# Kernel tuning notes

Hardware: AMD Instinct MI355X
Metric: run time of the kernel (lower is better)

## Reference

```python
import jax, jax.numpy as jnp
import numpy as np
from functools import partial

ZONEOUT = 0.1  # eval-mode zoneout: h = h_new + zr*(h_prev - h_new)


def gru_layer(x, h0, kernel, recurrent, bias, zr):
    """Keras v2 GRU (reset_after=True), gate order [z, r, h].
    x: [B,T,D], h0: [B,U], kernel: [D,3U], recurrent: [U,3U], bias: [2,3U].
    Returns pre-zoneout outputs [B,T,U]; zoneout applies only to the carried state."""
    U = h0.shape[-1]
    b_in, b_rec = bias[0], bias[1]
    # precompute input projection for all timesteps (the compute-heavy GEMM)
    xw = jnp.einsum('btd,dk->btk', x, kernel) + b_in  # [B,T,3U]

    def step(h, xw_t):
        m = h @ recurrent + b_rec                      # [B,3U]
        xz, xr, xh = xw_t[:, :U], xw_t[:, U:2 * U], xw_t[:, 2 * U:]
        mz, mr, mh = m[:, :U], m[:, U:2 * U], m[:, 2 * U:]
        z = jax.nn.sigmoid(xz + mz)
        r = jax.nn.sigmoid(xr + mr)
        hh = jnp.tanh(xh + r * mh)
        h_new = z * h + (1.0 - z) * hh                 # cell output
        h_carry = h_new + zr * (h - h_new)             # eval zoneout on state
        return h_carry, h_new

    _, ys = jax.lax.scan(step, h0, jnp.swapaxes(xw, 0, 1))  # scan over T
    return jnp.swapaxes(ys, 0, 1)  # [B,T,U]


def setup_inputs() -> dict:
    key = jax.random.key(0)
    ks = jax.random.split(key, 16)
    B, T, D, U = 32, 1024, 256, 512
    s_in, s_rec = 1.0 / np.sqrt(D), 1.0 / np.sqrt(U)
    return {
        'x':   jax.random.normal(ks[0], (B, T, D), jnp.float32),
        'k0':  jax.random.normal(ks[1], (D, 3 * U), jnp.float32) * s_in,
        'r0':  jax.random.normal(ks[2], (U, 3 * U), jnp.float32) * s_rec,
        'b0':  jnp.zeros((2, 3 * U), jnp.float32),
        'ks':  jax.random.normal(ks[3], (U, 3 * U), jnp.float32) * s_rec,
        'rs':  jax.random.normal(ks[4], (U, 3 * U), jnp.float32) * s_rec,
        'bs':  jnp.zeros((2, 3 * U), jnp.float32),
        'h00': jax.random.normal(ks[5], (1, U), jnp.float32),
        'h01': jax.random.normal(ks[6], (1, U), jnp.float32),
        'h02': jax.random.normal(ks[7], (1, U), jnp.float32),
        'a':   jnp.ones((3,), jnp.float32),  # scalar skip multipliers a_11, a_12, a_22
        'wd':  jax.random.normal(ks[8], (U, D), jnp.float32) * s_rec,
        'bd':  jnp.zeros((D,), jnp.float32),
    }


def reference(x, k0, r0, b0, ks, rs, bs, h00, h01, h02, a, wd, bd):
    B = x.shape[0]
    tile = lambda h: jnp.tile(h, (B, 1))  # learnable init state -> batch
    # layer 0
    out0 = gru_layer(x, tile(h00), k0, r0, b0, ZONEOUT)
    # RK-style skip connections with a SHARED cell but per-layer learnable init states
    h0_skip = [tile(h01), tile(h02)]
    intermediates = []
    x_cur = out0
    idx = 0
    for i in range(2):  # num_skip_connections = num_rnn_layers - 1 = 2
        pred = gru_layer(x_cur, h0_skip[i], ks, rs, bs, ZONEOUT)
        intermediates.append(pred)
        x_cur = out0
        for j in range(i + 1):
            x_cur = x_cur + a[idx] * intermediates[j]
            idx += 1
    # dense output head (linear)
    return jnp.einsum('btu,ud->btd', x_cur, wd) + bd
```

## Files before the change

### kernel.cpp

```cpp
#include <hip/hip_runtime.h>

typedef __attribute__((ext_vector_type(8))) short short8;
typedef __attribute__((ext_vector_type(4))) float f32x4;
typedef __attribute__((ext_vector_type(4))) unsigned short u16x4;
typedef unsigned short ushort;
typedef unsigned long long ull;

#define MFMA16(a,b,c) __builtin_amdgcn_mfma_f32_16x16x32_bf16((a),(b),(c),0,0,0)

static __device__ __forceinline__ float bf2f(ushort u){
  union { unsigned int i; float f; } z; z.i = ((unsigned int)u) << 16; return z.f;
}
static __device__ __forceinline__ ushort f2bf(float f){
  union { float f; unsigned int i; } z; z.f = f;
  unsigned int x = z.i;
  unsigned int r = (x + 0x7fffu + ((x >> 16) & 1u)) >> 16;
  return (ushort)r;
}

static __device__ __forceinline__ float ld_ring_bf(const ushort* base, int idx){
  const unsigned int* p = (const unsigned int*)(base + (idx & ~1));
  unsigned int w = __hip_atomic_load(p, __ATOMIC_RELAXED, __HIP_MEMORY_SCOPE_AGENT);
  return bf2f((idx & 1) ? (ushort)(w >> 16) : (ushort)(w & 0xffffu));
}
static __device__ __forceinline__ void st_hc2(ushort* p, ushort v){
  unsigned int vv = v;
  asm volatile("global_store_short %0, %1, off sc0 sc1" :: "v"(p), "v"(vv) : "memory");
}
static __device__ __forceinline__ void st_hc8(ushort* p, ull v){
  asm volatile("global_store_dwordx2 %0, %1, off sc0 sc1" :: "v"(p), "v"(v) : "memory");
}

static __device__ __forceinline__ void ld_frag16(const ushort* p, short8* o){
  asm volatile(
    "global_load_dwordx4 %0, %16, off sc0 sc1\n\t"
    "global_load_dwordx4 %1, %16, off offset:64 sc0 sc1\n\t"
    "global_load_dwordx4 %2, %16, off offset:128 sc0 sc1\n\t"
    "global_load_dwordx4 %3, %16, off offset:192 sc0 sc1\n\t"
    "global_load_dwordx4 %4, %16, off offset:256 sc0 sc1\n\t"
    "global_load_dwordx4 %5, %16, off offset:320 sc0 sc1\n\t"
    "global_load_dwordx4 %6, %16, off offset:384 sc0 sc1\n\t"
    "global_load_dwordx4 %7, %16, off offset:448 sc0 sc1\n\t"
    "global_load_dwordx4 %8, %16, off offset:512 sc0 sc1\n\t"
    "global_load_dwordx4 %9, %16, off offset:576 sc0 sc1\n\t"
    "global_load_dwordx4 %10, %16, off offset:640 sc0 sc1\n\t"
    "global_load_dwordx4 %11, %16, off offset:704 sc0 sc1\n\t"
    "global_load_dwordx4 %12, %16, off offset:768 sc0 sc1\n\t"
    "global_load_dwordx4 %13, %16, off offset:832 sc0 sc1\n\t"
    "global_load_dwordx4 %14, %16, off offset:896 sc0 sc1\n\t"
    "global_load_dwordx4 %15, %16, off offset:960 sc0 sc1\n\t"
    "s_waitcnt vmcnt(0)"
    : "=&v"(o[0]), "=&v"(o[1]), "=&v"(o[2]), "=&v"(o[3]),
      "=&v"(o[4]), "=&v"(o[5]), "=&v"(o[6]), "=&v"(o[7]),
      "=&v"(o[8]), "=&v"(o[9]), "=&v"(o[10]), "=&v"(o[11]),
      "=&v"(o[12]), "=&v"(o[13]), "=&v"(o[14]), "=&v"(o[15])
    : "v"(p)
    : "memory");
  __builtin_amdgcn_sched_barrier(0);
}

static __device__ __forceinline__ void ld_frag32(const ushort* pa, const ushort* pb,
                                                 short8* oa, short8* ob){
  asm volatile(
    "global_load_dwordx4 %0, %32, off sc0 sc1\n\t"
    "global_load_dwordx4 %1, %32, off offset:64 sc0 sc1\n\t"
    "global_load_dwordx4 %2, %32, off offset:128 sc0 sc1\n\t"
    "global_load_dwordx4 %3, %32, off offset:192 sc0 sc1\n\t"
    "global_load_dwordx4 %4, %32, off offset:256 sc0 sc1\n\t"
    "global_load_dwordx4 %5, %32, off offset:320 sc0 sc1\n\t"
    "global_load_dwordx4 %6, %32, off offset:384 sc0 sc1\n\t"
    "global_load_dwordx4 %7, %32, off offset:448 sc0 sc1\n\t"
    "global_load_dwordx4 %8, %32, off offset:512 sc0 sc1\n\t"
    "global_load_dwordx4 %9, %32, off offset:576 sc0 sc1\n\t"
    "global_load_dwordx4 %10, %32, off offset:640 sc0 sc1\n\t"
    "global_load_dwordx4 %11, %32, off offset:704 sc0 sc1\n\t"
    "global_load_dwordx4 %12, %32, off offset:768 sc0 sc1\n\t"
    "global_load_dwordx4 %13, %32, off offset:832 sc0 sc1\n\t"
    "global_load_dwordx4 %14, %32, off offset:896 sc0 sc1\n\t"
    "global_load_dwordx4 %15, %32, off offset:960 sc0 sc1\n\t"
    "global_load_dwordx4 %16, %33, off sc0 sc1\n\t"
    "global_load_dwordx4 %17, %33, off offset:64 sc0 sc1\n\t"
    "global_load_dwordx4 %18, %33, off offset:128 sc0 sc1\n\t"
    "global_load_dwordx4 %19, %33, off offset:192 sc0 sc1\n\t"
    "global_load_dwordx4 %20, %33, off offset:256 sc0 sc1\n\t"
    "global_load_dwordx4 %21, %33, off offset:320 sc0 sc1\n\t"
    "global_load_dwordx4 %22, %33, off offset:384 sc0 sc1\n\t"
    "global_load_dwordx4 %23, %33, off offset:448 sc0 sc1\n\t"
    "global_load_dwordx4 %24, %33, off offset:512 sc0 sc1\n\t"
    "global_load_dwordx4 %25, %33, off offset:576 sc0 sc1\n\t"
    "global_load_dwordx4 %26, %33, off offset:640 sc0 sc1\n\t"
    "global_load_dwordx4 %27, %33, off offset:704 sc0 sc1\n\t"
    "global_load_dwordx4 %28, %33, off offset:768 sc0 sc1\n\t"
    "global_load_dwordx4 %29, %33, off offset:832 sc0 sc1\n\t"
    "global_load_dwordx4 %30, %33, off offset:896 sc0 sc1\n\t"
    "global_load_dwordx4 %31, %33, off offset:960 sc0 sc1\n\t"
    "s_waitcnt vmcnt(0)"
    : "=&v"(oa[0]), "=&v"(oa[1]), "=&v"(oa[2]), "=&v"(oa[3]),
      "=&v"(oa[4]), "=&v"(oa[5]), "=&v"(oa[6]), "=&v"(oa[7]),
      "=&v"(oa[8]), "=&v"(oa[9]), "=&v"(oa[10]), "=&v"(oa[11]),
      "=&v"(oa[12]), "=&v"(oa[13]), "=&v"(oa[14]), "=&v"(oa[15]),
      "=&v"(ob[0]), "=&v"(ob[1]), "=&v"(ob[2]), "=&v"(ob[3]),
      "=&v"(ob[4]), "=&v"(ob[5]), "=&v"(ob[6]), "=&v"(ob[7]),
      "=&v"(ob[8]), "=&v"(ob[9]), "=&v"(ob[10]), "=&v"(ob[11]),
      "=&v"(ob[12]), "=&v"(ob[13]), "=&v"(ob[14]), "=&v"(ob[15])
    : "v"(pa), "v"(pb)
    : "memory");
  __builtin_amdgcn_sched_barrier(0);
}

static __device__ __forceinline__ void ld_frag32s(
    const ushort* pa, const ushort* pb,
    const ushort* q0, const ushort* q1, const ushort* q2,
    const ushort* q3, const ushort* q4, const ushort* q5,
    short8* oa, short8* ob,
    unsigned int* s0, unsigned int* s1, ull* s2,
    unsigned int* s3, unsigned int* s4, ull* s5)
{
  asm volatile(
    "global_load_dwordx4 %0, %38, off sc0 sc1\n\t"
    "global_load_dwordx4 %1, %38, off offset:64 sc0 sc1\n\t"
    "global_load_dwordx4 %2, %38, off offset:128 sc0 sc1\n\t"
    "global_load_dwordx4 %3, %38, off offset:192 sc0 sc1\n\t"
    "global_load_dwordx4 %4, %38, off offset:256 sc0 sc1\n\t"
    "global_load_dwordx4 %5, %38, off offset:320 sc0 sc1\n\t"
    "global_load_dwordx4 %6, %38, off offset:384 sc0 sc1\n\t"
    "global_load_dwordx4 %7, %38, off offset:448 sc0 sc1\n\t"
    "global_load_dwordx4 %8, %38, off offset:512 sc0 sc1\n\t"
    "global_load_dwordx4 %9, %38, off offset:576 sc0 sc1\n\t"
    "global_load_dwordx4 %10, %38, off offset:640 sc0 sc1\n\t"
    "global_load_dwordx4 %11, %38, off offset:704 sc0 sc1\n\t"
    "global_load_dwordx4 %12, %38, off offset:768 sc0 sc1\n\t"
    "global_load_dwordx4 %13, %38, off offset:832 sc0 sc1\n\t"
    "global_load_dwordx4 %14, %38, off offset:896 sc0 sc1\n\t"
    "global_load_dwordx4 %15, %38, off offset:960 sc0 sc1\n\t"
    "global_load_dwordx4 %16, %39, off sc0 sc1\n\t"
    "global_load_dwordx4 %17, %39, off offset:64 sc0 sc1\n\t"
    "global_load_dwordx4 %18, %39, off offset:128 sc0 sc1\n\t"
    "global_load_dwordx4 %19, %39, off offset:192 sc0 sc1\n\t"
    "global_load_dwordx4 %20, %39, off offset:256 sc0 sc1\n\t"
    "global_load_dwordx4 %21, %39, off offset:320 sc0 sc1\n\t"
    "global_load_dwordx4 %22, %39, off offset:384 sc0 sc1\n\t"
    "global_load_dwordx4 %23, %39, off offset:448 sc0 sc1\n\t"
    "global_load_dwordx4 %24, %39, off offset:512 sc0 sc1\n\t"
    "global_load_dwordx4 %25, %39, off offset:576 sc0 sc1\n\t"
    "global_load_dwordx4 %26, %39, off offset:640 sc0 sc1\n\t"
    "global_load_dwordx4 %27, %39, off offset:704 sc0 sc1\n\t"
    "global_load_dwordx4 %28, %39, off offset:768 sc0 sc1\n\t"
    "global_load_dwordx4 %29, %39, off offset:832 sc0 sc1\n\t"
    "global_load_dwordx4 %30, %39, off offset:896 sc0 sc1\n\t"
    "global_load_dwordx4 %31, %39, off offset:960 sc0 sc1\n\t"
    "global_load_dword %32, %40, off sc0 sc1\n\t"
    "global_load_dword %33, %41, off sc0 sc1\n\t"
    "global_load_dwordx2 %34, %42, off sc0 sc1\n\t"
    "global_load_dword %35, %43, off sc0 sc1\n\t"
    "global_load_dword %36, %44, off sc0 sc1\n\t"
    "global_load_dwordx2 %37, %45, off sc0 sc1\n\t"
    "s_waitcnt vmcnt(0)"
    : "=&v"(oa[0]), "=&v"(oa[1]), "=&v"(oa[2]), "=&v"(oa[3]),
      "=&v"(oa[4]), "=&v"(oa[5]), "=&v"(oa[6]), "=&v"(oa[7]),
      "=&v"(oa[8]), "=&v"(oa[9]), "=&v"(oa[10]), "=&v"(oa[11]),
      "=&v"(oa[12]), "=&v"(oa[13]), "=&v"(oa[14]), "=&v"(oa[15]),
      "=&v"(ob[0]), "=&v"(ob[1]), "=&v"(ob[2]), "=&v"(ob[3]),
      "=&v"(ob[4]), "=&v"(ob[5]), "=&v"(ob[6]), "=&v"(ob[7]),
      "=&v"(ob[8]), "=&v"(ob[9]), "=&v"(ob[10]), "=&v"(ob[11]),
      "=&v"(ob[12]), "=&v"(ob[13]), "=&v"(ob[14]), "=&v"(ob[15]),
      "=&v"(*s0), "=&v"(*s1), "=&v"(*s2), "=&v"(*s3), "=&v"(*s4), "=&v"(*s5)
    : "v"(pa), "v"(pb), "v"(q0), "v"(q1), "v"(q2), "v"(q3), "v"(q4), "v"(q5)
    : "memory");
  __builtin_amdgcn_sched_barrier(0);
}

__global__ __launch_bounds__(256) void cvt_k(
    const float* __restrict__ in, ushort* __restrict__ out, int n)
{
  int i = (blockIdx.x * 256 + threadIdx.x) * 4;
  if (i < n){
    float4 v = *(const float4*)(in + i);
    u16x4 o = { f2bf(v.x), f2bf(v.y), f2bf(v.z), f2bf(v.w) };
    *(u16x4*)(out + i) = o;
  }
}

template<int F32OUT>
__global__ __launch_bounds__(256) void gemm_bias_k(
    const ushort* __restrict__ A,
    const ushort* __restrict__ B,
    const float*  __restrict__ bias,
    void* __restrict__ Cv,
    int M, int N, int K)
{
  __shared__ __align__(16) ushort Blds[64 * 40];
  const int tid  = threadIdx.x;
  const int wid  = tid >> 6;
  const int lane = tid & 63;
  const int quad = lane >> 4;
  const int lc   = lane & 15;
  const int nb   = N >> 6;
  const int bn   = (blockIdx.x % nb) << 6;
  const int bm   = (blockIdx.x / nb) << 6;

  const int sk  = tid >> 3;
  const int scg = tid & 7;

  f32x4 acc[4] = {{0,0,0,0},{0,0,0,0},{0,0,0,0},{0,0,0,0}};
  const int arow = bm + wid * 16 + lc;
  const ushort* aptr = A + (size_t)arow * K + quad * 8;

  for (int k0 = 0; k0 < K; k0 += 32){
    short8 bv = *(const short8*)(B + (size_t)(k0 + sk) * N + bn + (scg << 3));
    #pragma unroll
    for (int i = 0; i < 8; ++i){
      int c = (scg << 3) + i;
      int p = c * 40 + (((sk >> 3) ^ (scg & 3)) << 3) + (sk & 7);
      Blds[p] = (ushort)bv[i];
    }
    __syncthreads();
    short8 av = *(const short8*)(aptr + k0);
    #pragma unroll
    for (int nt = 0; nt < 4; ++nt){
      int c2 = (nt << 4) + lc;
      int p  = c2 * 40 + ((quad ^ ((c2 >> 3) & 3)) << 3);
      short8 bfrag = *(const short8*)(Blds + p);
      acc[nt] = MFMA16(av, bfrag, acc[nt]);
    }
    __syncthreads();
  }
  #pragma unroll
  for (int nt = 0; nt < 4; ++nt){
    #pragma unroll
    for (int i = 0; i < 4; ++i){
      int m = bm + wid * 16 + quad * 4 + i;
      int n = bn + (nt << 4) + lc;
      float v = acc[nt][i] + bias[n];
      if (F32OUT) ((float*)Cv)[(size_t)m * N + n] = v;
      else        ((ushort*)Cv)[(size_t)m * N + n] = f2bf(v);
    }
  }
}

#define NWG 96
#define RD 8
#define FSTEPS 1032

__global__ __launch_bounds__(384, 1) void rec3_k(
    const ushort* __restrict__ xw0,
    const ushort* __restrict__ R0b,
    const ushort* __restrict__ Ksb,
    const ushort* __restrict__ Rsb,
    const float*  __restrict__ b0v,
    const float*  __restrict__ bsv,
    const float*  __restrict__ h00,
    const float*  __restrict__ h01,
    const float*  __restrict__ h02,
    const float*  __restrict__ av,
    ushort* __restrict__ comb,
    ushort* __restrict__ rings,
    int* __restrict__ flags)
{
  __shared__ float m_lds[3][32][17];
  __shared__ float x_lds[3][32][17];
  __shared__ float bias_l[96];
  __shared__ __align__(16) ushort ks_lds[3 * 16 * 64 * 8];
  __shared__ __align__(16) ushort rs_lds[3 * 16 * 64 * 8];

  const int tid  = threadIdx.x;
  const int wid  = tid >> 6;
  const int lane = tid & 63;
  const int quad = lane >> 4;
  const int lc   = lane & 15;
  const int bid  = blockIdx.x;
  const int role = bid >> 5;
  const int g    = bid & 31;
  const int ug0  = g << 4;
  const int gate = wid % 3, mtile = wid / 3;
  const int col0 = (gate << 9) + ug0;

  ushort* h_ring    = rings + role * 131072;
  ushort* out0ring  = rings + 393216;
  ushort* pred0ring = rings + 524288;
  ushort* xw1ring   = rings + 655360;

  short8 bfragR[16];
  if (role == 0){
    #pragma unroll
    for (int f = 0; f < 16; ++f){
      short8 v;
      #pragma unroll
      for (int j = 0; j < 8; ++j)
        v[j] = (short)R0b[(size_t)(f * 32 + quad * 8 + j) * 1536 + col0 + lc];
      bfragR[f] = v;
    }
  }
  if (role > 0){
    if (mtile == 0){
      #pragma unroll
      for (int f = 0; f < 16; ++f){
        short8 v;
        #pragma unroll
        for (int j = 0; j < 8; ++j)
          v[j] = (short)Ksb[(size_t)(f * 32 + quad * 8 + j) * 1536 + col0 + lc];
        *(short8*)(ks_lds + (((gate << 4) + f) << 9) + (lane << 3)) = v;
      }
    } else {
      #pragma unroll
      for (int f = 0; f < 16; ++f){
        short8 v;
        #pragma unroll
        for (int j = 0; j < 8; ++j)
          v[j] = (short)Rsb[(size_t)(f * 32 + quad * 8 + j) * 1536 + col0 + lc];
        *(short8*)(rs_lds + (((gate << 4) + f) << 9) + (lane << 3)) = v;
      }
    }
  }
  const float* brec = ((role == 0) ? b0v : bsv) + 1536;
  if (tid < 48) bias_l[tid] = brec[(tid >> 4) * 512 + ug0 + (tid & 15)];
  if (tid >= 48 && tid < 96) bias_l[tid] = bsv[((tid - 48) >> 4) * 512 + ug0 + ((tid - 48) & 15)];
  const float a0 = av[0], a1 = av[1], a2 = av[2];
  const float* hinit = (role == 0) ? h00 : (role == 1) ? h01 : h02;

  const int  b0i  = tid >> 4;
  const int  u0   = tid & 15;
  const int  b1i  = (tid + 384) >> 4;
  const bool has1 = (tid < 128);
  const int  uu   = ug0 + u0;
  float hp0 = hinit[uu];
  float hp1 = hp0;

  ushort xz0 = 0, xr0 = 0, xh0 = 0, xz1 = 0, xr1 = 0, xh1 = 0;
  if (role == 0){
    size_t r0_ = ((size_t)b0i * 1024) * 1536 + uu;
    xz0 = xw0[r0_]; xr0 = xw0[r0_ + 512]; xh0 = xw0[r0_ + 1024];
    if (has1){
      size_t r1_ = ((size_t)b1i * 1024) * 1536 + uu;
      xz1 = xw0[r1_]; xr1 = xw0[r1_ + 512]; xh1 = xw0[r1_ + 1024];
    }
  }
  __syncthreads();

  long budget = 40000000L;
  for (int t = 0; t < 1024; ++t){
    const int s     = t + role;
    const int slot  = t & (RD - 1);
    const int pslot = (t - 1) & (RD - 1);

    ushort nz0 = 0, nr0 = 0, nh0 = 0, nz1 = 0, nr1 = 0, nh1 = 0;
    if (role == 0 && t < 1023){
      size_t r0_ = ((size_t)b0i * 1024 + t + 1) * 1536 + uu;
      nz0 = xw0[r0_]; nr0 = xw0[r0_ + 512]; nh0 = xw0[r0_ + 1024];
      if (has1){
        size_t r1_ = ((size_t)b1i * 1024 + t + 1) * 1536 + uu;
        nz1 = xw0[r1_]; nr1 = xw0[r1_ + 512]; nh1 = xw0[r1_ + 1024];
      }
    }

    {
      const bool needO = (t > 0);
      const bool needP = (role >= 1);
      const bool needF = (role <= 1) && (s >= RD);
      if ((needO || needP || needF) && wid == 0){
        const int  l    = lane & 31;
        const int* fo   = flags + (role * FSTEPS + (s - 1)) * 32 + l;
        const int* fp   = flags + ((role - 1) * FSTEPS + (s - 1)) * 32 + l;
        const int* ff   = flags + (2 * FSTEPS + (s - 6)) * 32 + l;
        while (budget > 0){
          bool ok = true;
          if (needO) ok &= (__hip_atomic_load(fo, __ATOMIC_RELAXED, __HIP_MEMORY_SCOPE_AGENT) != 0);
          if (needP) ok &= (__hip_atomic_load(fp, __ATOMIC_RELAXED, __HIP_MEMORY_SCOPE_AGENT) != 0);
          if (needF) ok &= (__hip_atomic_load(ff, __ATOMIC_RELAXED, __HIP_MEMORY_SCOPE_AGENT) != 0);
          if (__ballot(ok) == ~0ull) break;
          --budget;
        }
      }
      __syncthreads();
    }

    float o_s0 = 0, p_s0 = 0, x1z0 = 0, x1r0 = 0, x1h0 = 0;
    float o_s1 = 0, p_s1 = 0, x1z1 = 0, x1r1 = 0, x1h1 = 0;
    {
      short8 avm[16];
      short8 avx[16];
      const ushort* hr  = h_ring + pslot * 16384 + (mtile * 16 + lc) * 512 + quad * 8;
      const ushort* xr_ = ((role == 1) ? out0ring : pred0ring)
                        + slot * 16384 + (mtile * 16 + lc) * 512 + quad * 8;

      if (t == 0){
        #pragma unroll
        for (int f = 0; f < 16; ++f){
          short8 v;
          #pragma unroll
          for (int j = 0; j < 8; ++j)
            v[j] = (short)f2bf(hinit[f * 32 + quad * 8 + j]);
          avm[f] = v;
        }
        if (role >= 1) ld_frag16(xr_, avx);
        if (role == 2){
          int rb0 = slot * 16384 + b0i * 512 + uu;
          o_s0 = ld_ring_bf(out0ring, rb0);
          p_s0 = ld_ring_bf(pred0ring, rb0);
          ull xwp = __hip_atomic_load((const ull*)(xw1ring + (size_t)((slot * 32 + b0i) * 512 + uu) * 4),
                                      __ATOMIC_RELAXED, __HIP_MEMORY_SCOPE_AGENT);
          x1z0 = bf2f((ushort)(xwp & 0xffffu));
          x1r0 = bf2f((ushort)((xwp >> 16) & 0xffffu));
          x1h0 = bf2f((ushort)((xwp >> 32) & 0xffffu));
          if (has1){
            int rb1 = slot * 16384 + b1i * 512 + uu;
            o_s1 = ld_ring_bf(out0ring, rb1);
            p_s1 = ld_ring_bf(pred0ring, rb1);
            ull xwq = __hip_atomic_load((const ull*)(xw1ring + (size_t)((slot * 32 + b1i) * 512 + uu) * 4),
                                        __ATOMIC_RELAXED, __HIP_MEMORY_SCOPE_AGENT);
            x1z1 = bf2f((ushort)(xwq & 0xffffu));
            x1r1 = bf2f((ushort)((xwq >> 16) & 0xffffu));
            x1h1 = bf2f((ushort)((xwq >> 32) & 0xffffu));
          }
        }
      } else if (role == 0){
        ld_frag16(hr, avm);
      } else if (role == 1){
        ld_frag32(xr_, hr, avx, avm);
      } else {
        int rb0 = slot * 16384 + b0i * 512 + uu;
        int rb1 = slot * 16384 + b1i * 512 + uu;
        const ushort* q0 = out0ring  + (rb0 & ~1);
        const ushort* q1 = pred0ring + (rb0 & ~1);
        const ushort* q2 = xw1ring + (size_t)((slot * 32 + b0i) * 512 + uu) * 4;
        const ushort* q3 = has1 ? (out0ring  + (rb1 & ~1)) : q0;
        const ushort* q4 = has1 ? (pred0ring + (rb1 & ~1)) : q1;
        const ushort* q5 = has1 ? (xw1ring + (size_t)((slot * 32 + b1i) * 512 + uu) * 4) : q2;
        unsigned int w0, w1, w3, w4; ull w2, w5;
        ld_frag32s(xr_, hr, q0, q1, q2, q3, q4, q5,
                   avx, avm, &w0, &w1, &w2, &w3, &w4, &w5);
        int hi = uu & 1;
        o_s0 = bf2f(hi ? (ushort)(w0 >> 16) : (ushort)(w0 & 0xffffu));
        p_s0 = bf2f(hi ? (ushort)(w1 >> 16) : (ushort)(w1 & 0xffffu));
        x1z0 = bf2f((ushort)(w2 & 0xffffu));
        x1r0 = bf2f((ushort)((w2 >> 16) & 0xffffu));
        x1h0 = bf2f((ushort)((w2 >> 32) & 0xffffu));
        if (has1){
          o_s1 = bf2f(hi ? (ushort)(w3 >> 16) : (ushort)(w3 & 0xffffu));
          p_s1 = bf2f(hi ? (ushort)(w4 >> 16) : (ushort)(w4 & 0xffffu));
          x1z1 = bf2f((ushort)(w5 & 0xffffu));
          x1r1 = bf2f((ushort)((w5 >> 16) & 0xffffu));
          x1h1 = bf2f((ushort)((w5 >> 32) & 0xffffu));
        }
      }

      f32x4 am0 = {0,0,0,0}, am1 = {0,0,0,0};
      if (role == 0){
        #pragma unroll
        for (int f = 0; f < 16; ++f){
          if (f & 1) am1 = MFMA16(avm[f], bfragR[f], am1);
          else       am0 = MFMA16(avm[f], bfragR[f], am0);
        }
        f32x4 am = am0 + am1;
        #pragma unroll
        for (int i = 0; i < 4; ++i)
          m_lds[gate][(mtile << 4) + (quad << 2) + i][lc] = am[i];
      } else {
        f32x4 ax0 = {0,0,0,0}, ax1 = {0,0,0,0};
        #pragma unroll
        for (int f = 0; f < 16; ++f){
          short8 bx = *(const short8*)(ks_lds + (((gate << 4) + f) << 9) + (lane << 3));
          short8 br = *(const short8*)(rs_lds + (((gate << 4) + f) << 9) + (lane << 3));
          if (f & 1){ am1 = MFMA16(avm[f], br, am1); ax1 = MFMA16(avx[f], bx, ax1); }
          else      { am0 = MFMA16(avm[f], br, am0); ax0 = MFMA16(avx[f], bx, ax0); }
        }
        f32x4 am = am0 + am1, ax = ax0 + ax1;
        #pragma unroll
        for (int i = 0; i < 4; ++i){
          m_lds[gate][(mtile << 4) + (quad << 2) + i][lc] = am[i];
          x_lds[gate][(mtile << 4) + (quad << 2) + i][lc] = ax[i];
        }
      }
    }
    __syncthreads();

    ushort cb0 = 0, cb1 = 0;
    {
      int b = b0i;
      float mz = m_lds[0][b][u0] + bias_l[u0];
      float mr = m_lds[1][b][u0] + bias_l[16 + u0];
      float mh = m_lds[2][b][u0] + bias_l[32 + u0];
      float xz, xr, xh;
      if (role == 0){ xz = bf2f(xz0); xr = bf2f(xr0); xh = bf2f(xh0); }
      else if (role == 1){
        xz = x_lds[0][b][u0] + bias_l[48 + u0];
        xr = x_lds[1][b][u0] + bias_l[64 + u0];
        xh = x_lds[2][b][u0] + bias_l[80 + u0];
      } else {
        xz = x1z0 + a0 * x_lds[0][b][u0] + bias_l[48 + u0];
        xr = x1r0 + a0 * x_lds[1][b][u0] + bias_l[64 + u0];
        xh = x1h0 + a0 * x_lds[2][b][u0] + bias_l[80 + u0];
      }
      float z  = 1.f / (1.f + __expf(-(xz + mz)));
      float r  = 1.f / (1.f + __expf(-(xr + mr)));
      float axv = xh + r * mh;
      float hh = 1.f - 2.f / (1.f + __expf(2.f * axv));
      float hn = z * hp0 + (1.f - z) * hh;
      float hcv = hn + 0.1f * (hp0 - hn);
      hp0 = hcv;
      int rb = slot * 16384 + b * 512 + uu;
      st_hc2(h_ring + rb, f2bf(hcv));
      if (role == 0) st_hc2(out0ring + rb, f2bf(hn));
      else if (role == 1){
        st_hc2(pred0ring + rb, f2bf(hn));
        ull pv = (ull)f2bf(x_lds[0][b][u0])
               | ((ull)f2bf(x_lds[1][b][u0]) << 16)
               | ((ull)f2bf(x_lds[2][b][u0]) << 32);
        st_hc8(xw1ring + (size_t)((slot * 32 + b) * 512 + uu) * 4, pv);
      } else {
        cb0 = f2bf(o_s0 + a1 * p_s0 + a2 * hn);
      }
    }
    if (has1){
      int b = b1i;
      float mz = m_lds[0][b][u0] + bias_l[u0];
      float mr = m_lds[1][b][u0] + bias_l[16 + u0];
      float mh = m_lds[2][b][u0] + bias_l[32 + u0];
      float xz, xr, xh;
      if (role == 0){ xz = bf2f(xz1); xr = bf2f(xr1); xh = bf2f(xh1); }
      else if (role == 1){
        xz = x_lds[0][b][u0] + bias_l[48 + u0];
        xr = x_lds[1][b][u0] + bias_l[64 + u0];
        xh = x_lds[2][b][u0] + bias_l[80 + u0];
      } else {
        xz = x1z1 + a0 * x_lds[0][b][u0] + bias_l[48 + u0];
        xr = x1r1 + a0 * x_lds[1][b][u0] + bias_l[64 + u0];
        xh = x1h1 + a0 * x_lds[2][b][u0] + bias_l[80 + u0];
      }
      float z  = 1.f / (1.f + __expf(-(xz + mz)));
      float r  = 1.f / (1.f + __expf(-(xr + mr)));
      float axv = xh + r * mh;
      float hh = 1.f - 2.f / (1.f + __expf(2.f * axv));
      float hn = z * hp1 + (1.f - z) * hh;
      float hcv = hn + 0.1f * (hp1 - hn);
      hp1 = hcv;
      int rb = slot * 16384 + b * 512 + uu;
      st_hc2(h_ring + rb, f2bf(hcv));
      if (role == 0) st_hc2(out0ring + rb, f2bf(hn));
      else if (role == 1){
        st_hc2(pred0ring + rb, f2bf(hn));
        ull pv = (ull)f2bf(x_lds[0][b][u0])
               | ((ull)f2bf(x_lds[1][b][u0]) << 16)
               | ((ull)f2bf(x_lds[2][b][u0]) << 32);
        st_hc8(xw1ring + (size_t)((slot * 32 + b) * 512 + uu) * 4, pv);
      } else {
        cb1 = f2bf(o_s1 + a1 * p_s1 + a2 * hn);
      }
    }
    asm volatile("s_waitcnt vmcnt(0)" ::: "memory");
    __syncthreads();
    if (tid == 0)
      __hip_atomic_store(flags + (role * FSTEPS + s) * 32 + g, 1,
                         __ATOMIC_RELAXED, __HIP_MEMORY_SCOPE_AGENT);
    if (role == 2){
      comb[((size_t)b0i * 1024 + t) * 512 + uu] = cb0;
      if (has1) comb[((size_t)b1i * 1024 + t) * 512 + uu] = cb1;
    }

    if (role == 0){
      xz0 = nz0; xr0 = nr0; xh0 = nh0;
      xz1 = nz1; xr1 = nr1; xh1 = nh1;
    }
  }
}

extern "C" void kernel_launch(void* const* d_in, const int* in_sizes, int n_in,
                              void* d_out, int out_size, void* d_ws, size_t ws_size,
                              hipStream_t stream)
{
  const float* x   = (const float*)d_in[0];
  const float* k0  = (const float*)d_in[1];
  const float* r0  = (const float*)d_in[2];
  const float* b0  = (const float*)d_in[3];
  const float* ks  = (const float*)d_in[4];
  const float* rs  = (const float*)d_in[5];
  const float* bs  = (const float*)d_in[6];
  const float* h00 = (const float*)d_in[7];
  const float* h01 = (const float*)d_in[8];
  const float* h02 = (const float*)d_in[9];
  const float* a   = (const float*)d_in[10];
  const float* wd  = (const float*)d_in[11];
  const float* bd  = (const float*)d_in[12];
  float* outp = (float*)d_out;

  char* ws = (char*)d_ws;
  ushort* XW    = (ushort*)(ws);
  ushort* combp = (ushort*)(ws + 100663296u);
  ushort* xbf   = combp;
  ushort* rings = (ushort*)(ws + 134217728u);
  int*    flags = (int*)   (ws + 136577024u);
  ushort* k0b   = (ushort*)(ws + 136973312u);
  ushort* r0b   = (ushort*)(ws + 137759744u);
  ushort* ksb   = (ushort*)(ws + 139332608u);
  ushort* rsb   = (ushort*)(ws + 140905472u);
  ushort* wdb   = (ushort*)(ws + 142478336u);

  hipMemsetAsync(flags, 0, 3 * FSTEPS * 32 * sizeof(int), stream);

  dim3 blk(256);
  cvt_k<<<dim3(8192), blk, 0, stream>>>(x,  xbf, 8388608);
  cvt_k<<<dim3(384),  blk, 0, stream>>>(k0, k0b, 393216);
  cvt_k<<<dim3(768),  blk, 0, stream>>>(r0, r0b, 786432);
  cvt_k<<<dim3(768),  blk, 0, stream>>>(ks, ksb, 786432);
  cvt_k<<<dim3(768),  blk, 0, stream>>>(rs, rsb, 786432);
  cvt_k<<<dim3(128),  blk, 0, stream>>>(wd, wdb, 131072);

  gemm_bias_k<0><<<dim3(512 * 24), blk, 0, stream>>>(xbf, k0b, b0, XW, 32768, 1536, 256);
  rec3_k<<<dim3(NWG), dim3(384), 0, stream>>>(XW, r0b, ksb, rsb, b0, bs,
                                              h00, h01, h02, a, combp, rings, flags);
  gemm_bias_k<1><<<dim3(512 * 4), blk, 0, stream>>>(combp, wdb, bd, outp, 32768, 256, 512);
}
```

Before: 10.48 ms.

## Split recurrence flags into h-state and cross-layer sets, publish h early

The per-step flags change from one-shot booleans over all steps to monotonic step counters in a 64-entry ring, in two separate sets. One set signals that the carried h state is ready, the other that the cross-layer outputs (out0, pred0, xw1) are ready. Each workgroup now stores and publishes its h_ring slice first, then writes the cross-layer rings and raises a second flag, so same-role neighbours can start the next step sooner. All waves poll the flags instead of only wave 0, and the __syncthreads after the wait is removed. The cost is an extra vmcnt wait and barrier per step for roles 0 and 1, and reliance on every wave seeing the flags consistently without a barrier.

```diff
diff --git a/kernel.cpp b/kernel.cpp
--- a/kernel.cpp
+++ b/kernel.cpp
@@ -240,7 +240,6 @@
 
 #define NWG 96
 #define RD 8
-#define FSTEPS 1032
 
 __global__ __launch_bounds__(384, 1) void rec3_k(
     const ushort* __restrict__ xw0,
@@ -275,6 +274,9 @@
   const int gate = wid % 3, mtile = wid / 3;
   const int col0 = (gate << 9) + ug0;
 
+  int* flagsH = flags;
+  int* flagsX = flags + 6144;
+
   ushort* h_ring    = rings + role * 131072;
   ushort* out0ring  = rings + 393216;
   ushort* pred0ring = rings + 524288;
@@ -357,21 +359,20 @@
       const bool needO = (t > 0);
       const bool needP = (role >= 1);
       const bool needF = (role <= 1) && (s >= RD);
-      if ((needO || needP || needF) && wid == 0){
-        const int  l    = lane & 31;
-        const int* fo   = flags + (role * FSTEPS + (s - 1)) * 32 + l;
-        const int* fp   = flags + ((role - 1) * FSTEPS + (s - 1)) * 32 + l;
-        const int* ff   = flags + (2 * FSTEPS + (s - 6)) * 32 + l;
+      if (needO || needP || needF){
+        const int  l  = lane & 31;
+        const int* fo = flagsH + ((role << 6) + ((s - 1) & 63)) * 32 + l;
+        const int* fp = flagsX + (((role - 1) << 6) + ((s - 1) & 63)) * 32 + l;
+        const int* ff = flagsH + ((2 << 6) + ((s - 6) & 63)) * 32 + l;
         while (budget > 0){
           bool ok = true;
-          if (needO) ok &= (__hip_atomic_load(fo, __ATOMIC_RELAXED, __HIP_MEMORY_SCOPE_AGENT) != 0);
-          if (needP) ok &= (__hip_atomic_load(fp, __ATOMIC_RELAXED, __HIP_MEMORY_SCOPE_AGENT) != 0);
-          if (needF) ok &= (__hip_atomic_load(ff, __ATOMIC_RELAXED, __HIP_MEMORY_SCOPE_AGENT) != 0);
+          if (needO) ok &= (__hip_atomic_load(fo, __ATOMIC_RELAXED, __HIP_MEMORY_SCOPE_AGENT) >= s);
+          if (needP) ok &= (__hip_atomic_load(fp, __ATOMIC_RELAXED, __HIP_MEMORY_SCOPE_AGENT) >= s);
+          if (needF) ok &= (__hip_atomic_load(ff, __ATOMIC_RELAXED, __HIP_MEMORY_SCOPE_AGENT) >= s - 5);
           if (__ballot(ok) == ~0ull) break;
           --budget;
         }
       }
-      __syncthreads();
     }
 
     float o_s0 = 0, p_s0 = 0, x1z0 = 0, x1r0 = 0, x1h0 = 0;
@@ -474,6 +475,8 @@
     }
     __syncthreads();
 
+    float hn0v = 0.f, hn1v = 0.f;
+    ull   pv0 = 0, pv1 = 0;
     ushort cb0 = 0, cb1 = 0;
     {
       int b = b0i;
@@ -483,9 +486,11 @@
       float xz, xr, xh;
       if (role == 0){ xz = bf2f(xz0); xr = bf2f(xr0); xh = bf2f(xh0); }
       else if (role == 1){
-        xz = x_lds[0][b][u0] + bias_l[48 + u0];
-        xr = x_lds[1][b][u0] + bias_l[64 + u0];
-        xh = x_lds[2][b][u0] + bias_l[80 + u0];
+        float wz = x_lds[0][b][u0], wr = x_lds[1][b][u0], wh = x_lds[2][b][u0];
+        pv0 = (ull)f2bf(wz) | ((ull)f2bf(wr) << 16) | ((ull)f2bf(wh) << 32);
+        xz = wz + bias_l[48 + u0];
+        xr = wr + bias_l[64 + u0];
+        xh = wh + bias_l[80 + u0];
       } else {
         xz = x1z0 + a0 * x_lds[0][b][u0] + bias_l[48 + u0];
         xr = x1r0 + a0 * x_lds[1][b][u0] + bias_l[64 + u0];
@@ -497,19 +502,9 @@
       float hh = 1.f - 2.f / (1.f + __expf(2.f * axv));
       float hn = z * hp0 + (1.f - z) * hh;
       float hcv = hn + 0.1f * (hp0 - hn);
-      hp0 = hcv;
-      int rb = slot * 16384 + b * 512 + uu;
-      st_hc2(h_ring + rb, f2bf(hcv));
-      if (role == 0) st_hc2(out0ring + rb, f2bf(hn));
-      else if (role == 1){
-        st_hc2(pred0ring + rb, f2bf(hn));
-        ull pv = (ull)f2bf(x_lds[0][b][u0])
-               | ((ull)f2bf(x_lds[1][b][u0]) << 16)
-               | ((ull)f2bf(x_lds[2][b][u0]) << 32);
-        st_hc8(xw1ring + (size_t)((slot * 32 + b) * 512 + uu) * 4, pv);
-      } else {
-        cb0 = f2bf(o_s0 + a1 * p_s0 + a2 * hn);
-      }
+      hp0 = hcv; hn0v = hn;
+      st_hc2(h_ring + slot * 16384 + b * 512 + uu, f2bf(hcv));
+      if (role == 2) cb0 = f2bf(o_s0 + a1 * p_s0 + a2 * hn);
     }
     if (has1){
       int b = b1i;
@@ -519,9 +514,11 @@
       float xz, xr, xh;
       if (role == 0){ xz = bf2f(xz1); xr = bf2f(xr1); xh = bf2f(xh1); }
       else if (role == 1){
-        xz = x_lds[0][b][u0] + bias_l[48 + u0];
-        xr = x_lds[1][b][u0] + bias_l[64 + u0];
-        xh = x_lds[2][b][u0] + bias_l[80 + u0];
+        float wz = x_lds[0][b][u0], wr = x_lds[1][b][u0], wh = x_lds[2][b][u0];
+        pv1 = (ull)f2bf(wz) | ((ull)f2bf(wr) << 16) | ((ull)f2bf(wh) << 32);
+        xz = wz + bias_l[48 + u0];
+        xr = wr + bias_l[64 + u0];
+        xh = wh + bias_l[80 + u0];
       } else {
         xz = x1z1 + a0 * x_lds[0][b][u0] + bias_l[48 + u0];
         xr = x1r1 + a0 * x_lds[1][b][u0] + bias_l[64 + u0];
@@ -533,26 +530,38 @@
       float hh = 1.f - 2.f / (1.f + __expf(2.f * axv));
       float hn = z * hp1 + (1.f - z) * hh;
       float hcv = hn + 0.1f * (hp1 - hn);
-      hp1 = hcv;
-      int rb = slot * 16384 + b * 512 + uu;
-      st_hc2(h_ring + rb, f2bf(hcv));
-      if (role == 0) st_hc2(out0ring + rb, f2bf(hn));
-      else if (role == 1){
-        st_hc2(pred0ring + rb, f2bf(hn));
-        ull pv = (ull)f2bf(x_lds[0][b][u0])
-               | ((ull)f2bf(x_lds[1][b][u0]) << 16)
-               | ((ull)f2bf(x_lds[2][b][u0]) << 32);
-        st_hc8(xw1ring + (size_t)((slot * 32 + b) * 512 + uu) * 4, pv);
-      } else {
-        cb1 = f2bf(o_s1 + a1 * p_s1 + a2 * hn);
-      }
-    }
+      hp1 = hcv; hn1v = hn;
+      st_hc2(h_ring + slot * 16384 + b * 512 + uu, f2bf(hcv));
+      if (role == 2) cb1 = f2bf(o_s1 + a1 * p_s1 + a2 * hn);
+    }
+
     asm volatile("s_waitcnt vmcnt(0)" ::: "memory");
     __syncthreads();
     if (tid == 0)
-      __hip_atomic_store(flags + (role * FSTEPS + s) * 32 + g, 1,
+      __hip_atomic_store(flagsH + ((role << 6) + (s & 63)) * 32 + g, s + 1,
                          __ATOMIC_RELAXED, __HIP_MEMORY_SCOPE_AGENT);
-    if (role == 2){
+
+    if (role == 0){
+      st_hc2(out0ring + slot * 16384 + b0i * 512 + uu, f2bf(hn0v));
+      if (has1) st_hc2(out0ring + slot * 16384 + b1i * 512 + uu, f2bf(hn1v));
+      asm volatile("s_waitcnt vmcnt(0)" ::: "memory");
+      __syncthreads();
+      if (tid == 0)
+        __hip_atomic_store(flagsX + ((s & 63)) * 32 + g, s + 1,
+                           __ATOMIC_RELAXED, __HIP_MEMORY_SCOPE_AGENT);
+    } else if (role == 1){
+      st_hc2(pred0ring + slot * 16384 + b0i * 512 + uu, f2bf(hn0v));
+      st_hc8(xw1ring + (size_t)((slot * 32 + b0i) * 512 + uu) * 4, pv0);
+      if (has1){
+        st_hc2(pred0ring + slot * 16384 + b1i * 512 + uu, f2bf(hn1v));
+        st_hc8(xw1ring + (size_t)((slot * 32 + b1i) * 512 + uu) * 4, pv1);
+      }
+      asm volatile("s_waitcnt vmcnt(0)" ::: "memory");
+      __syncthreads();
+      if (tid == 0)
+        __hip_atomic_store(flagsX + ((1 << 6) + (s & 63)) * 32 + g, s + 1,
+                           __ATOMIC_RELAXED, __HIP_MEMORY_SCOPE_AGENT);
+    } else {
       comb[((size_t)b0i * 1024 + t) * 512 + uu] = cb0;
       if (has1) comb[((size_t)b1i * 1024 + t) * 512 + uu] = cb1;
     }
@@ -595,7 +604,7 @@
   ushort* rsb   = (ushort*)(ws + 140905472u);
   ushort* wdb   = (ushort*)(ws + 142478336u);
 
-  hipMemsetAsync(flags, 0, 3 * FSTEPS * 32 * sizeof(int), stream);
+  hipMemsetAsync(flags, 0, 2 * 3 * 64 * 32 * sizeof(int), stream);
 
   dim3 blk(256);
   cvt_k<<<dim3(8192), blk, 0, stream>>>(x,  xbf, 8388608);
```

After: 10.99 ms. +4.9%, slower.
